# Kernel optimization log

Hardware: AMD Instinct MI355X
Metric: run time of the kernel (lower is better)

Reference implementation:

```python
import jax, jax.numpy as jnp
import numpy as np

N, C, E = 100000, 128, 600000
H = C // 2  # 64


def setup_inputs() -> dict:
    key = jax.random.key(0)
    k1, k2, k3, k4, k5, k6, k7, k8 = jax.random.split(key, 8)
    z_in = jax.random.normal(k1, (N, C), dtype=jnp.float32)
    z_out = jax.random.normal(k2, (N, C), dtype=jnp.float32)
    z_self = jax.random.normal(k3, (N, C), dtype=jnp.float32)
    edge_index = jax.random.randint(k4, (2, E), 0, N, dtype=jnp.int64)
    # MLP params: Linear(C, C//2) -> ELU -> (Dropout eval=no-op) -> Linear(C//2, 1)
    lim1 = 1.0 / np.sqrt(C)
    W1 = jax.random.uniform(k5, (C, H), minval=-lim1, maxval=lim1, dtype=jnp.float32)
    b1 = jax.random.uniform(k6, (H,), minval=-lim1, maxval=lim1, dtype=jnp.float32)
    lim2 = 1.0 / np.sqrt(H)
    W2 = jax.random.uniform(k7, (H, 1), minval=-lim2, maxval=lim2, dtype=jnp.float32)
    b2 = jax.random.uniform(k8, (1,), minval=-lim2, maxval=lim2, dtype=jnp.float32)
    return {"z_in": z_in, "z_out": z_out, "z_self": z_self,
            "edge_index": edge_index, "W1": W1, "b1": b1, "W2": W2, "b2": b2}


def reference(z_in, z_out, z_self, edge_index, W1, b1, W2, b2):
    v1 = z_out + z_self                       # [N, C]
    v2 = z_in + z_self                        # [N, C]
    value = v1[edge_index[0]] * v2[edge_index[1]]  # [E, C] gather + elementwise product
    h = jax.nn.elu(value @ W1 + b1)           # [E, H]; dropout is identity at eval
    logits = h @ W2 + b2                      # [E, 1]
    return jax.nn.sigmoid(logits)
```

## Files before the change

### kernel.cpp

```cpp
#include <hip/hip_runtime.h>
#include <hip/hip_bf16.h>

typedef __attribute__((ext_vector_type(8))) short short8;
typedef __attribute__((ext_vector_type(4))) float f32x4;

__device__ __forceinline__ unsigned short f2bf(float f) {
    unsigned u = __float_as_uint(f);
    u += 0x7fffu + ((u >> 16) & 1u);
    return (unsigned short)(u >> 16);
}

__device__ __forceinline__ unsigned bfmul_trunc(unsigned a, unsigned b) {
    float al = __uint_as_float(a << 16);
    float ah = __uint_as_float(a & 0xffff0000u);
    float bl = __uint_as_float(b << 16);
    float bh = __uint_as_float(b & 0xffff0000u);
    unsigned pl = __float_as_uint(al * bl);
    unsigned ph = __float_as_uint(ah * bh);
    return __builtin_amdgcn_perm(ph, pl, 0x07060302u);
}

__device__ __forceinline__ unsigned pack_trunc(float lo, float hi) {
    return __builtin_amdgcn_perm(__float_as_uint(hi), __float_as_uint(lo), 0x07060302u);
}

__global__ __launch_bounds__(256) void prep_kernel(
    const f32x4* __restrict__ zin, const f32x4* __restrict__ zout,
    const f32x4* __restrict__ zself,
    ushort4* __restrict__ v1b, ushort4* __restrict__ v2b, int n4)
{
    const int base = blockIdx.x * 1024 + threadIdx.x;
    const bool full = (blockIdx.x + 1) * 1024 <= n4;
    if (full) {
        f32x4 o[4], s[4], z[4];
#pragma unroll
        for (int u = 0; u < 4; u++) {
            const int i = base + u * 256;
            o[u] = __builtin_nontemporal_load(zout + i);
            s[u] = __builtin_nontemporal_load(zself + i);
            z[u] = __builtin_nontemporal_load(zin + i);
        }
#pragma unroll
        for (int u = 0; u < 4; u++) {
            const int i = base + u * 256;
            ushort4 a, b;
            a.x = f2bf(o[u].x + s[u].x); a.y = f2bf(o[u].y + s[u].y);
            a.z = f2bf(o[u].z + s[u].z); a.w = f2bf(o[u].w + s[u].w);
            b.x = f2bf(z[u].x + s[u].x); b.y = f2bf(z[u].y + s[u].y);
            b.z = f2bf(z[u].z + s[u].z); b.w = f2bf(z[u].w + s[u].w);
            v1b[i] = a; v2b[i] = b;
        }
    } else {
#pragma unroll
        for (int u = 0; u < 4; u++) {
            const int i = base + u * 256;
            if (i < n4) {
                f32x4 o = __builtin_nontemporal_load(zout + i);
                f32x4 s = __builtin_nontemporal_load(zself + i);
                f32x4 z = __builtin_nontemporal_load(zin + i);
                ushort4 a, b;
                a.x = f2bf(o.x + s.x); a.y = f2bf(o.y + s.y);
                a.z = f2bf(o.z + s.z); a.w = f2bf(o.w + s.w);
                b.x = f2bf(z.x + s.x); b.y = f2bf(z.y + s.y);
                b.z = f2bf(z.z + s.z); b.w = f2bf(z.w + s.w);
                v1b[i] = a; v2b[i] = b;
            }
        }
    }
}

__global__ __launch_bounds__(256, 4) void edge_pipe(
    const unsigned short* __restrict__ v1b, const unsigned short* __restrict__ v2b,
    const int* __restrict__ idx,
    const float* __restrict__ W1, const float* __restrict__ b1,
    const float* __restrict__ W2, const float* __restrict__ b2,
    float* __restrict__ out, int E, int ntiles)
{
    __shared__ __align__(16) unsigned short ldsW[16 * 64 * 8];

    const int tid  = threadIdx.x;
    const int wave = tid >> 6;
    const int lane = tid & 63;
    const int nn = lane & 15;
    const int q  = lane >> 4;

#pragma unroll
    for (int i = 0; i < 4; i++) {
        int p = tid * 4 + i;
        int f = p >> 6, l = p & 63;
        int kc = f >> 2, jt = f & 3, lq = (l >> 4) & 3, ln = l & 15;
        const float* wp = W1 + (size_t)(kc * 32 + lq * 8) * 64 + jt * 16 + ln;
        uint4 wv;
        wv.x = (unsigned)f2bf(wp[0 * 64]) | ((unsigned)f2bf(wp[1 * 64]) << 16);
        wv.y = (unsigned)f2bf(wp[2 * 64]) | ((unsigned)f2bf(wp[3 * 64]) << 16);
        wv.z = (unsigned)f2bf(wp[4 * 64]) | ((unsigned)f2bf(wp[5 * 64]) << 16);
        wv.w = (unsigned)f2bf(wp[6 * 64]) | ((unsigned)f2bf(wp[7 * 64]) << 16);
        *(uint4*)&ldsW[p * 8] = wv;
    }
    __syncthreads();

    float bias1[4], w2v[4];
#pragma unroll
    for (int jt = 0; jt < 4; jt++) {
        bias1[jt] = b1[jt * 16 + nn];
        w2v[jt]   = W2[jt * 16 + nn];
    }
    const float b2v = b2[0];

    const int nwaves = gridDim.x * 4;
    int tile = blockIdx.x * 4 + wave;
    if (tile >= ntiles) return;
    const int* __restrict__ idxE = idx + E;

    const int e0  = min(tile * 16 + nn, E - 1);
    const int t1  = tile + nwaves;
    const int tc1 = (t1 < ntiles) ? t1 : tile;
    const int e1  = min(tc1 * 16 + nn, E - 1);
    const int src0 = __builtin_nontemporal_load(idx  + e0);
    const int dst0 = __builtin_nontemporal_load(idxE + e0);
    int srcn = __builtin_nontemporal_load(idx  + e1);
    int dstn = __builtin_nontemporal_load(idxE + e1);

    uint4 a[4], b[4];
    {
        const uint4* p1 = (const uint4*)(v1b + (size_t)src0 * 128);
        const uint4* p2 = (const uint4*)(v2b + (size_t)dst0 * 128);
#pragma unroll
        for (int kc = 0; kc < 4; kc++) { a[kc] = p1[kc * 4 + q]; b[kc] = p2[kc * 4 + q]; }
    }

    for (; tile < ntiles; tile += nwaves) {
        const int t2  = tile + 2 * nwaves;
        const int tc2 = (t2 < ntiles) ? t2 : tile;
        const int e2  = min(tc2 * 16 + nn, E - 1);
        const int src2 = __builtin_nontemporal_load(idx  + e2);
        const int dst2 = __builtin_nontemporal_load(idxE + e2);

        short8 Af[4];
#pragma unroll
        for (int kc = 0; kc < 4; kc++) {
            uint4 p;
            p.x = bfmul_trunc(a[kc].x, b[kc].x);
            p.y = bfmul_trunc(a[kc].y, b[kc].y);
            p.z = bfmul_trunc(a[kc].z, b[kc].z);
            p.w = bfmul_trunc(a[kc].w, b[kc].w);
            Af[kc] = __builtin_bit_cast(short8, p);
        }

        {
            const uint4* p1 = (const uint4*)(v1b + (size_t)srcn * 128);
            const uint4* p2 = (const uint4*)(v2b + (size_t)dstn * 128);
#pragma unroll
            for (int kc = 0; kc < 4; kc++) { a[kc] = p1[kc * 4 + q]; b[kc] = p2[kc * 4 + q]; }
        }
        srcn = src2; dstn = dst2;

        f32x4 acc[4];
#pragma unroll
        for (int jt = 0; jt < 4; jt++) acc[jt] = (f32x4){0.f, 0.f, 0.f, 0.f};
#pragma unroll
        for (int kc = 0; kc < 4; kc++) {
#pragma unroll
            for (int jt = 0; jt < 4; jt++) {
                short8 Bf = *(const short8*)&ldsW[((kc * 4 + jt) * 64 + lane) * 8];
                acc[jt] = __builtin_amdgcn_mfma_f32_16x16x32_bf16(Af[kc], Bf, acc[jt], 0, 0, 0);
            }
        }

        float ps[4];
#pragma unroll
        for (int r = 0; r < 4; r++) {
            float s = 0.f;
#pragma unroll
            for (int jt = 0; jt < 4; jt++) {
                float h = acc[jt][r] + bias1[jt];
                h = (h > 0.f) ? h : (__expf(h) - 1.f);
                s += h * w2v[jt];
            }
            ps[r] = s;
        }
#pragma unroll
        for (int off = 1; off < 16; off <<= 1) {
#pragma unroll
            for (int r = 0; r < 4; r++)
                ps[r] += __shfl_xor(ps[r], off, 64);
        }
        if (nn == 0) {
#pragma unroll
            for (int r = 0; r < 4; r++) {
                int e = tile * 16 + q * 4 + r;
                if (e < E) {
                    float x = ps[r] + b2v;
                    __builtin_nontemporal_store(1.f / (1.f + __expf(-x)), out + e);
                }
            }
        }
    }
}

__global__ __launch_bounds__(256) void edge_f32(
    const float* __restrict__ zin, const float* __restrict__ zout,
    const float* __restrict__ zself,
    const int* __restrict__ idx,
    const float* __restrict__ W1, const float* __restrict__ b1,
    const float* __restrict__ W2, const float* __restrict__ b2,
    float* __restrict__ out, int E, int ntiles)
{
    const int wave = threadIdx.x >> 6;
    const int lane = threadIdx.x & 63;
    const int nn = lane & 15;
    const int q  = lane >> 4;

    short8 Bf[4][4];
#pragma unroll
    for (int kc = 0; kc < 4; kc++)
#pragma unroll
        for (int jt = 0; jt < 4; jt++) {
            short8 v;
#pragma unroll
            for (int t = 0; t < 8; t++)
                v[t] = (short)f2bf(W1[(kc * 32 + q * 8 + t) * 64 + jt * 16 + nn]);
            Bf[kc][jt] = v;
        }
    float bias1[4], w2v[4];
#pragma unroll
    for (int jt = 0; jt < 4; jt++) {
        bias1[jt] = b1[jt * 16 + nn];
        w2v[jt]   = W2[jt * 16 + nn];
    }
    const float b2v = b2[0];

    const int nwaves = gridDim.x * 4;
    for (int tile = blockIdx.x * 4 + wave; tile < ntiles; tile += nwaves) {
        const int ebase = tile * 16;
        const int ee  = min(ebase + nn, E - 1);
        const int src = idx[ee];
        const int dst = idx[E + ee];

        short8 Af[4];
        const float* po  = zout  + (size_t)src * 128 + q * 8;
        const float* ps1 = zself + (size_t)src * 128 + q * 8;
        const float* pi  = zin   + (size_t)dst * 128 + q * 8;
        const float* ps2 = zself + (size_t)dst * 128 + q * 8;
#pragma unroll
        for (int kc = 0; kc < 4; kc++) {
            float4 oa = *(const float4*)(po  + kc * 32), ob = *(const float4*)(po  + kc * 32 + 4);
            float4 sa = *(const float4*)(ps1 + kc * 32), sb = *(const float4*)(ps1 + kc * 32 + 4);
            float4 ia = *(const float4*)(pi  + kc * 32), ib = *(const float4*)(pi  + kc * 32 + 4);
            float4 ta = *(const float4*)(ps2 + kc * 32), tb = *(const float4*)(ps2 + kc * 32 + 4);
            uint4 p;
            p.x = pack_trunc((oa.x + sa.x) * (ia.x + ta.x), (oa.y + sa.y) * (ia.y + ta.y));
            p.y = pack_trunc((oa.z + sa.z) * (ia.z + ta.z), (oa.w + sa.w) * (ia.w + ta.w));
            p.z = pack_trunc((ob.x + sb.x) * (ib.x + tb.x), (ob.y + sb.y) * (ib.y + tb.y));
            p.w = pack_trunc((ob.z + sb.z) * (ib.z + tb.z), (ob.w + sb.w) * (ib.w + tb.w));
            Af[kc] = __builtin_bit_cast(short8, p);
        }

        f32x4 acc[4];
#pragma unroll
        for (int jt = 0; jt < 4; jt++) acc[jt] = (f32x4){0.f, 0.f, 0.f, 0.f};
#pragma unroll
        for (int kc = 0; kc < 4; kc++)
#pragma unroll
            for (int jt = 0; jt < 4; jt++)
                acc[jt] = __builtin_amdgcn_mfma_f32_16x16x32_bf16(Af[kc], Bf[kc][jt], acc[jt], 0, 0, 0);

        float ps[4];
#pragma unroll
        for (int r = 0; r < 4; r++) {
            float s = 0.f;
#pragma unroll
            for (int jt = 0; jt < 4; jt++) {
                float h = acc[jt][r] + bias1[jt];
                h = (h > 0.f) ? h : (__expf(h) - 1.f);
                s += h * w2v[jt];
            }
            ps[r] = s;
        }
#pragma unroll
        for (int off = 1; off < 16; off <<= 1) {
#pragma unroll
            for (int r = 0; r < 4; r++)
                ps[r] += __shfl_xor(ps[r], off, 64);
        }
        if (nn == 0) {
#pragma unroll
            for (int r = 0; r < 4; r++) {
                int e = ebase + q * 4 + r;
                if (e < E) {
                    float x = ps[r] + b2v;
                    out[e] = 1.f / (1.f + __expf(-x));
                }
            }
        }
    }
}

extern "C" void kernel_launch(void* const* d_in, const int* in_sizes, int n_in,
                              void* d_out, int out_size, void* d_ws, size_t ws_size,
                              hipStream_t stream)
{
    const float* zin   = (const float*)d_in[0];
    const float* zout  = (const float*)d_in[1];
    const float* zself = (const float*)d_in[2];
    const int*   idx   = (const int*)d_in[3];
    const float* W1    = (const float*)d_in[4];
    const float* b1    = (const float*)d_in[5];
    const float* W2    = (const float*)d_in[6];
    const float* b2    = (const float*)d_in[7];
    float* out = (float*)d_out;

    const int NC = in_sizes[0];
    const int E  = in_sizes[3] / 2;
    const int ntiles = (E + 15) / 16;
    const size_t need = (size_t)NC * 4;

    if (ws_size >= need) {
        unsigned short* v1b = (unsigned short*)d_ws;
        unsigned short* v2b = v1b + NC;
        const int n4 = NC / 4;
        const int nblocks = (n4 + 1023) / 1024;
        prep_kernel<<<nblocks, 256, 0, stream>>>(
            (const f32x4*)zin, (const f32x4*)zout, (const f32x4*)zself,
            (ushort4*)v1b, (ushort4*)v2b, n4);

        const int cap = 2048;
        int iters = (ntiles + cap * 4 - 1) / (cap * 4);
        if (iters < 1) iters = 1;
        int eblocks = (ntiles + iters * 4 - 1) / (iters * 4);
        edge_pipe<<<eblocks, 256, 0, stream>>>(
            v1b, v2b, idx, W1, b1, W2, b2, out, E, ntiles);
    } else {
        edge_f32<<<2048, 256, 0, stream>>>(
            zin, zout, zself, idx, W1, b1, W2, b2, out, E, ntiles);
    }
}
```

Baseline: 225.9 us.

## Bucket edges by source node range before gathering to improve cache locality

Adds a scatter pass that partitions edges into 16 buckets by source-node range, writing (src, dst, edge id) records. The edge kernel then assigns blocks to buckets so that concurrently running waves gather from a narrower slice of v1b, aiming for better L2/MALL reuse. Outputs are written back through the stored edge id. The cost is two extra kernel launches, an extra read of the indices, a 16-byte-per-edge record write and read, and scattered output stores.

```diff
diff --git a/kernel.cpp b/kernel.cpp
--- a/kernel.cpp
+++ b/kernel.cpp
@@ -3,6 +3,9 @@
 
 typedef __attribute__((ext_vector_type(8))) short short8;
 typedef __attribute__((ext_vector_type(4))) float f32x4;
+typedef __attribute__((ext_vector_type(4))) int   i32x4;
+
+#define NBKT 16
 
 __device__ __forceinline__ unsigned short f2bf(float f) {
     unsigned u = __float_as_uint(f);
@@ -69,12 +72,47 @@
     }
 }
 
-__global__ __launch_bounds__(256, 4) void edge_pipe(
+__global__ void k_init(int* ctl, int cap)
+{
+    if (threadIdx.x < NBKT) ctl[threadIdx.x] = threadIdx.x * cap;
+}
+
+__global__ __launch_bounds__(256) void k_scatter(
+    const int* __restrict__ idx, int E, int slice, int CH,
+    int* __restrict__ ctl, int cap, i32x4* __restrict__ rec)
+{
+    __shared__ int hist[NBKT], base[NBKT];
+    const int c0 = blockIdx.x * CH;
+    const int c1 = min(c0 + CH, E);
+    if (threadIdx.x < NBKT) hist[threadIdx.x] = 0;
+    __syncthreads();
+    for (int e = c0 + threadIdx.x; e < c1; e += 256) {
+        int b = min(idx[e] / slice, NBKT - 1);
+        atomicAdd(&hist[b], 1);
+    }
+    __syncthreads();
+    if (threadIdx.x < NBKT) {
+        int c = hist[threadIdx.x];
+        base[threadIdx.x] = c ? atomicAdd(&ctl[threadIdx.x], c)
+                              : threadIdx.x * cap;
+        hist[threadIdx.x] = 0;
+    }
+    __syncthreads();
+    for (int e = c0 + threadIdx.x; e < c1; e += 256) {
+        int s = idx[e], d = idx[E + e];
+        int b = min(s / slice, NBKT - 1);
+        int p = base[b] + atomicAdd(&hist[b], 1);
+        i32x4 r; r[0] = s; r[1] = d; r[2] = e; r[3] = 0;
+        __builtin_nontemporal_store(r, rec + p);
+    }
+}
+
+__global__ __launch_bounds__(256, 4) void edge_bkt(
     const unsigned short* __restrict__ v1b, const unsigned short* __restrict__ v2b,
-    const int* __restrict__ idx,
+    const i32x4* __restrict__ rec, const int* __restrict__ ctl, int cap,
     const float* __restrict__ W1, const float* __restrict__ b1,
     const float* __restrict__ W2, const float* __restrict__ b2,
-    float* __restrict__ out, int E, int ntiles)
+    float* __restrict__ out)
 {
     __shared__ __align__(16) unsigned short ldsW[16 * 64 * 8];
 
@@ -107,6 +145,144 @@
     }
     const float b2v = b2[0];
 
+    const int nw  = (gridDim.x >> 3) * 4;
+    const int wi0 = (blockIdx.x >> 3) * 4 + wave;
+    const int bkt0 = blockIdx.x & 7;
+
+    for (int ph = 0; ph < 2; ph++) {
+        const int bk = bkt0 + ph * 8;
+        const int bbase = bk * cap;
+        const int bcnt  = ctl[bk] - bbase;
+        const int btiles = (bcnt + 15) >> 4;
+        int t = ph ? (nw - 1 - wi0) : wi0;
+        if (t >= btiles) continue;
+
+        auto recAt = [&](int tt) -> i32x4 {
+            int r = min(tt * 16 + nn, bcnt - 1);
+            return __builtin_nontemporal_load(rec + bbase + r);
+        };
+
+        i32x4 r0 = recAt(t);
+        const int tA = t + nw;
+        i32x4 r1 = recAt(tA < btiles ? tA : t);
+        int eo_cur = r0[2];
+        int srcn = r1[0], dstn = r1[1], eon = r1[2];
+
+        uint4 a[4], b[4];
+        {
+            const uint4* p1 = (const uint4*)(v1b + (size_t)r0[0] * 128);
+            const uint4* p2 = (const uint4*)(v2b + (size_t)r0[1] * 128);
+#pragma unroll
+            for (int kc = 0; kc < 4; kc++) { a[kc] = p1[kc * 4 + q]; b[kc] = p2[kc * 4 + q]; }
+        }
+
+        for (; t < btiles; t += nw) {
+            const int t2 = t + 2 * nw;
+            i32x4 r2 = recAt(t2 < btiles ? t2 : t);
+
+            short8 Af[4];
+#pragma unroll
+            for (int kc = 0; kc < 4; kc++) {
+                uint4 p;
+                p.x = bfmul_trunc(a[kc].x, b[kc].x);
+                p.y = bfmul_trunc(a[kc].y, b[kc].y);
+                p.z = bfmul_trunc(a[kc].z, b[kc].z);
+                p.w = bfmul_trunc(a[kc].w, b[kc].w);
+                Af[kc] = __builtin_bit_cast(short8, p);
+            }
+
+            {
+                const uint4* p1 = (const uint4*)(v1b + (size_t)srcn * 128);
+                const uint4* p2 = (const uint4*)(v2b + (size_t)dstn * 128);
+#pragma unroll
+                for (int kc = 0; kc < 4; kc++) { a[kc] = p1[kc * 4 + q]; b[kc] = p2[kc * 4 + q]; }
+            }
+            const int eo_st = eo_cur;
+            eo_cur = eon;
+            srcn = r2[0]; dstn = r2[1]; eon = r2[2];
+
+            f32x4 acc[4];
+#pragma unroll
+            for (int jt = 0; jt < 4; jt++) acc[jt] = (f32x4){0.f, 0.f, 0.f, 0.f};
+#pragma unroll
+            for (int kc = 0; kc < 4; kc++) {
+#pragma unroll
+                for (int jt = 0; jt < 4; jt++) {
+                    short8 Bf = *(const short8*)&ldsW[((kc * 4 + jt) * 64 + lane) * 8];
+                    acc[jt] = __builtin_amdgcn_mfma_f32_16x16x32_bf16(Af[kc], Bf, acc[jt], 0, 0, 0);
+                }
+            }
+
+            float ps[4];
+#pragma unroll
+            for (int r = 0; r < 4; r++) {
+                float s = 0.f;
+#pragma unroll
+                for (int jt = 0; jt < 4; jt++) {
+                    float h = acc[jt][r] + bias1[jt];
+                    h = (h > 0.f) ? h : (__expf(h) - 1.f);
+                    s += h * w2v[jt];
+                }
+                ps[r] = s;
+            }
+#pragma unroll
+            for (int off = 1; off < 16; off <<= 1) {
+#pragma unroll
+                for (int r = 0; r < 4; r++)
+                    ps[r] += __shfl_xor(ps[r], off, 64);
+            }
+            int eoq[4];
+#pragma unroll
+            for (int r = 0; r < 4; r++) eoq[r] = __shfl(eo_st, (q << 2) + r, 16);
+            if (nn == 0) {
+#pragma unroll
+                for (int r = 0; r < 4; r++) {
+                    float x = ps[r] + b2v;
+                    __builtin_nontemporal_store(1.f / (1.f + __expf(-x)), out + eoq[r]);
+                }
+            }
+        }
+    }
+}
+
+__global__ __launch_bounds__(256, 4) void edge_pipe(
+    const unsigned short* __restrict__ v1b, const unsigned short* __restrict__ v2b,
+    const int* __restrict__ idx,
+    const float* __restrict__ W1, const float* __restrict__ b1,
+    const float* __restrict__ W2, const float* __restrict__ b2,
+    float* __restrict__ out, int E, int ntiles)
+{
+    __shared__ __align__(16) unsigned short ldsW[16 * 64 * 8];
+
+    const int tid  = threadIdx.x;
+    const int wave = tid >> 6;
+    const int lane = tid & 63;
+    const int nn = lane & 15;
+    const int q  = lane >> 4;
+
+#pragma unroll
+    for (int i = 0; i < 4; i++) {
+        int p = tid * 4 + i;
+        int f = p >> 6, l = p & 63;
+        int kc = f >> 2, jt = f & 3, lq = (l >> 4) & 3, ln = l & 15;
+        const float* wp = W1 + (size_t)(kc * 32 + lq * 8) * 64 + jt * 16 + ln;
+        uint4 wv;
+        wv.x = (unsigned)f2bf(wp[0 * 64]) | ((unsigned)f2bf(wp[1 * 64]) << 16);
+        wv.y = (unsigned)f2bf(wp[2 * 64]) | ((unsigned)f2bf(wp[3 * 64]) << 16);
+        wv.z = (unsigned)f2bf(wp[4 * 64]) | ((unsigned)f2bf(wp[5 * 64]) << 16);
+        wv.w = (unsigned)f2bf(wp[6 * 64]) | ((unsigned)f2bf(wp[7 * 64]) << 16);
+        *(uint4*)&ldsW[p * 8] = wv;
+    }
+    __syncthreads();
+
+    float bias1[4], w2v[4];
+#pragma unroll
+    for (int jt = 0; jt < 4; jt++) {
+        bias1[jt] = b1[jt * 16 + nn];
+        w2v[jt]   = W2[jt * 16 + nn];
+    }
+    const float b2v = b2[0];
+
     const int nwaves = gridDim.x * 4;
     int tile = blockIdx.x * 4 + wave;
     if (tile >= ntiles) return;
@@ -146,7 +322,6 @@
             p.w = bfmul_trunc(a[kc].w, b[kc].w);
             Af[kc] = __builtin_bit_cast(short8, p);
         }
-
         {
             const uint4* p1 = (const uint4*)(v1b + (size_t)srcn * 128);
             const uint4* p2 = (const uint4*)(v2b + (size_t)dstn * 128);
@@ -312,20 +487,48 @@
 
     const int NC = in_sizes[0];
     const int E  = in_sizes[3] / 2;
+    const int N  = NC / 128;
     const int ntiles = (E + 15) / 16;
-    const size_t need = (size_t)NC * 4;
-
-    if (ws_size >= need) {
+
+    const int slice = (N + NBKT - 1) / NBKT;
+    const int cap   = E / NBKT + 2048;
+
+    const size_t need1 = (size_t)NC * 4;
+    const size_t off_rec = need1;
+    const size_t off_ctl = off_rec + (size_t)NBKT * cap * 16;
+    const size_t need2 = off_ctl + 256;
+
+    if (ws_size >= need2) {
+        unsigned short* v1b = (unsigned short*)d_ws;
+        unsigned short* v2b = v1b + NC;
+        i32x4* rec = (i32x4*)((char*)d_ws + off_rec);
+        int*   ctl = (int*)((char*)d_ws + off_ctl);
+        const int n4 = NC / 4;
+        prep_kernel<<<(n4 + 1023) / 1024, 256, 0, stream>>>(
+            (const f32x4*)zin, (const f32x4*)zout, (const f32x4*)zself,
+            (ushort4*)v1b, (ushort4*)v2b, n4);
+        k_init<<<1, 64, 0, stream>>>(ctl, cap);
+        const int SB = 256;
+        const int CH = (E + SB - 1) / SB;
+        k_scatter<<<SB, 256, 0, stream>>>(idx, E, slice, CH, ctl, cap, rec);
+
+        int iters = (ntiles + 8191) / 8192; if (iters < 1) iters = 1;
+        int nwavesT = (ntiles + iters - 1) / iters;
+        int wpg = (nwavesT + 7) / 8;
+        int bpg = (wpg + 3) / 4;
+        if (bpg < 1) bpg = 1;
+        if (bpg > 256) bpg = 256;
+        edge_bkt<<<bpg * 8, 256, 0, stream>>>(
+            v1b, v2b, rec, ctl, cap, W1, b1, W2, b2, out);
+    } else if (ws_size >= need1) {
         unsigned short* v1b = (unsigned short*)d_ws;
         unsigned short* v2b = v1b + NC;
         const int n4 = NC / 4;
-        const int nblocks = (n4 + 1023) / 1024;
-        prep_kernel<<<nblocks, 256, 0, stream>>>(
+        prep_kernel<<<(n4 + 1023) / 1024, 256, 0, stream>>>(
             (const f32x4*)zin, (const f32x4*)zout, (const f32x4*)zself,
             (ushort4*)v1b, (ushort4*)v2b, n4);
-
-        const int cap = 2048;
-        int iters = (ntiles + cap * 4 - 1) / (cap * 4);
+        const int cap2 = 2048;
+        int iters = (ntiles + cap2 * 4 - 1) / (cap2 * 4);
         if (iters < 1) iters = 1;
         int eblocks = (ntiles + iters * 4 - 1) / (iters * 4);
         edge_pipe<<<eblocks, 256, 0, stream>>>(
```

Result: slower. 263.2 us (+16.5%).

## Quantize node features to int8 with per-row scales to halve gather traffic

Applied to the files above, without the earlier changes.

The prep kernel now stores v1 and v2 as int8 with one absmax scale per row, instead of bf16. The edge kernel gathers 8-byte chunks instead of 16-byte chunks, plus two scale loads per edge. It then dequantizes each product as int8*int8*scale before packing to bf16 for the MFMA. This halves the random-gather bytes per edge and shrinks the prep kernel's writes, which matters because the random gathers dominate the cost. The trade-offs are more ALU work per element for unpacking and conversion, extra scalar scale loads, and lower precision from per-row 8-bit quantization.

```diff
diff --git a/kernel.cpp b/kernel.cpp
--- a/kernel.cpp
+++ b/kernel.cpp
@@ -10,67 +10,70 @@
     return (unsigned short)(u >> 16);
 }
 
-__device__ __forceinline__ unsigned bfmul_trunc(unsigned a, unsigned b) {
-    float al = __uint_as_float(a << 16);
-    float ah = __uint_as_float(a & 0xffff0000u);
-    float bl = __uint_as_float(b << 16);
-    float bh = __uint_as_float(b & 0xffff0000u);
-    unsigned pl = __float_as_uint(al * bl);
-    unsigned ph = __float_as_uint(ah * bh);
-    return __builtin_amdgcn_perm(ph, pl, 0x07060302u);
-}
-
 __device__ __forceinline__ unsigned pack_trunc(float lo, float hi) {
     return __builtin_amdgcn_perm(__float_as_uint(hi), __float_as_uint(lo), 0x07060302u);
 }
 
-__global__ __launch_bounds__(256) void prep_kernel(
+
+__global__ __launch_bounds__(256) void prep_i8(
     const f32x4* __restrict__ zin, const f32x4* __restrict__ zout,
     const f32x4* __restrict__ zself,
-    ushort4* __restrict__ v1b, ushort4* __restrict__ v2b, int n4)
+    unsigned* __restrict__ q1, unsigned* __restrict__ q2,
+    float* __restrict__ s1, float* __restrict__ s2, int N)
 {
-    const int base = blockIdx.x * 1024 + threadIdx.x;
-    const bool full = (blockIdx.x + 1) * 1024 <= n4;
-    if (full) {
-        f32x4 o[4], s[4], z[4];
-#pragma unroll
-        for (int u = 0; u < 4; u++) {
-            const int i = base + u * 256;
-            o[u] = __builtin_nontemporal_load(zout + i);
-            s[u] = __builtin_nontemporal_load(zself + i);
-            z[u] = __builtin_nontemporal_load(zin + i);
-        }
-#pragma unroll
-        for (int u = 0; u < 4; u++) {
-            const int i = base + u * 256;
-            ushort4 a, b;
-            a.x = f2bf(o[u].x + s[u].x); a.y = f2bf(o[u].y + s[u].y);
-            a.z = f2bf(o[u].z + s[u].z); a.w = f2bf(o[u].w + s[u].w);
-            b.x = f2bf(z[u].x + s[u].x); b.y = f2bf(z[u].y + s[u].y);
-            b.z = f2bf(z[u].z + s[u].z); b.w = f2bf(z[u].w + s[u].w);
-            v1b[i] = a; v2b[i] = b;
-        }
-    } else {
-#pragma unroll
-        for (int u = 0; u < 4; u++) {
-            const int i = base + u * 256;
-            if (i < n4) {
-                f32x4 o = __builtin_nontemporal_load(zout + i);
-                f32x4 s = __builtin_nontemporal_load(zself + i);
-                f32x4 z = __builtin_nontemporal_load(zin + i);
-                ushort4 a, b;
-                a.x = f2bf(o.x + s.x); a.y = f2bf(o.y + s.y);
-                a.z = f2bf(o.z + s.z); a.w = f2bf(o.w + s.w);
-                b.x = f2bf(z.x + s.x); b.y = f2bf(z.y + s.y);
-                b.z = f2bf(z.z + s.z); b.w = f2bf(z.w + s.w);
-                v1b[i] = a; v2b[i] = b;
-            }
-        }
-    }
-}
-
-__global__ __launch_bounds__(256, 4) void edge_pipe(
-    const unsigned short* __restrict__ v1b, const unsigned short* __restrict__ v2b,
+    const int lane = threadIdx.x & 63;
+    const int wave = threadIdx.x >> 6;
+    const int h    = lane >> 5;
+    const int l32  = lane & 31;
+    const int row  = blockIdx.x * 8 + wave * 2 + h;
+    if (row >= N) return;
+    const size_t rb = (size_t)row * 32 + l32;
+
+    f32x4 o = __builtin_nontemporal_load(zout  + rb);
+    f32x4 s = __builtin_nontemporal_load(zself + rb);
+    f32x4 z = __builtin_nontemporal_load(zin   + rb);
+    float v1[4] = {o.x + s.x, o.y + s.y, o.z + s.z, o.w + s.w};
+    float v2[4] = {z.x + s.x, z.y + s.y, z.z + s.z, z.w + s.w};
+
+    float m1 = fmaxf(fmaxf(fabsf(v1[0]), fabsf(v1[1])),
+                     fmaxf(fabsf(v1[2]), fabsf(v1[3])));
+    float m2 = fmaxf(fmaxf(fabsf(v2[0]), fabsf(v2[1])),
+                     fmaxf(fabsf(v2[2]), fabsf(v2[3])));
+#pragma unroll
+    for (int off = 1; off < 32; off <<= 1) {
+        m1 = fmaxf(m1, __shfl_xor(m1, off, 64));
+        m2 = fmaxf(m2, __shfl_xor(m2, off, 64));
+    }
+    m1 = fmaxf(m1, 1e-20f);
+    m2 = fmaxf(m2, 1e-20f);
+    const float i1 = 127.0f / m1, i2 = 127.0f / m2;
+
+    int qa[4], qb[4];
+#pragma unroll
+    for (int j = 0; j < 4; j++) {
+        qa[j] = (int)rintf(v1[j] * i1);
+        qb[j] = (int)rintf(v2[j] * i2);
+    }
+    unsigned wa = (unsigned)(qa[0] & 255) | ((unsigned)(qa[1] & 255) << 8) |
+                  ((unsigned)(qa[2] & 255) << 16) | ((unsigned)qa[3] << 24);
+    unsigned wb = (unsigned)(qb[0] & 255) | ((unsigned)(qb[1] & 255) << 8) |
+                  ((unsigned)(qb[2] & 255) << 16) | ((unsigned)qb[3] << 24);
+    q1[rb] = wa; q2[rb] = wb;
+    if (l32 == 0) {
+        s1[row] = m1 * (1.0f / 127.0f);
+        s2[row] = m2 * (1.0f / 127.0f);
+    }
+}
+
+__device__ __forceinline__ float pmul(unsigned aw, unsigned bw, int sh) {
+    int a = (int)(signed char)(aw >> sh);
+    int b = (int)(signed char)(bw >> sh);
+    return (float)(a * b);
+}
+
+__global__ __launch_bounds__(256, 4) void edge_pipe_i8(
+    const unsigned* __restrict__ q1, const unsigned* __restrict__ q2,
+    const float* __restrict__ s1, const float* __restrict__ s2,
     const int* __restrict__ idx,
     const float* __restrict__ W1, const float* __restrict__ b1,
     const float* __restrict__ W2, const float* __restrict__ b2,
@@ -121,10 +124,12 @@
     int srcn = __builtin_nontemporal_load(idx  + e1);
     int dstn = __builtin_nontemporal_load(idxE + e1);
 
-    uint4 a[4], b[4];
+    float sN_a = s1[src0], sN_b = s2[dst0];
+
+    uint2 a[4], b[4];
     {
-        const uint4* p1 = (const uint4*)(v1b + (size_t)src0 * 128);
-        const uint4* p2 = (const uint4*)(v2b + (size_t)dst0 * 128);
+        const uint2* p1 = (const uint2*)q1 + (size_t)src0 * 16;
+        const uint2* p2 = (const uint2*)q2 + (size_t)dst0 * 16;
 #pragma unroll
         for (int kc = 0; kc < 4; kc++) { a[kc] = p1[kc * 4 + q]; b[kc] = p2[kc * 4 + q]; }
     }
@@ -136,22 +141,28 @@
         const int src2 = __builtin_nontemporal_load(idx  + e2);
         const int dst2 = __builtin_nontemporal_load(idxE + e2);
 
+        const float s12 = sN_a * sN_b;
         short8 Af[4];
 #pragma unroll
         for (int kc = 0; kc < 4; kc++) {
             uint4 p;
-            p.x = bfmul_trunc(a[kc].x, b[kc].x);
-            p.y = bfmul_trunc(a[kc].y, b[kc].y);
-            p.z = bfmul_trunc(a[kc].z, b[kc].z);
-            p.w = bfmul_trunc(a[kc].w, b[kc].w);
+            p.x = pack_trunc(pmul(a[kc].x, b[kc].x,  0) * s12,
+                             pmul(a[kc].x, b[kc].x,  8) * s12);
+            p.y = pack_trunc(pmul(a[kc].x, b[kc].x, 16) * s12,
+                             pmul(a[kc].x, b[kc].x, 24) * s12);
+            p.z = pack_trunc(pmul(a[kc].y, b[kc].y,  0) * s12,
+                             pmul(a[kc].y, b[kc].y,  8) * s12);
+            p.w = pack_trunc(pmul(a[kc].y, b[kc].y, 16) * s12,
+                             pmul(a[kc].y, b[kc].y, 24) * s12);
             Af[kc] = __builtin_bit_cast(short8, p);
         }
 
         {
-            const uint4* p1 = (const uint4*)(v1b + (size_t)srcn * 128);
-            const uint4* p2 = (const uint4*)(v2b + (size_t)dstn * 128);
+            const uint2* p1 = (const uint2*)q1 + (size_t)srcn * 16;
+            const uint2* p2 = (const uint2*)q2 + (size_t)dstn * 16;
 #pragma unroll
             for (int kc = 0; kc < 4; kc++) { a[kc] = p1[kc * 4 + q]; b[kc] = p2[kc * 4 + q]; }
+            sN_a = s1[srcn]; sN_b = s2[dstn];
         }
         srcn = src2; dstn = dst2;
 
@@ -311,25 +322,26 @@
     float* out = (float*)d_out;
 
     const int NC = in_sizes[0];
+    const int N  = NC / 128;
     const int E  = in_sizes[3] / 2;
     const int ntiles = (E + 15) / 16;
-    const size_t need = (size_t)NC * 4;
+    const size_t need = (size_t)NC * 2 + (size_t)N * 8;
 
     if (ws_size >= need) {
-        unsigned short* v1b = (unsigned short*)d_ws;
-        unsigned short* v2b = v1b + NC;
-        const int n4 = NC / 4;
-        const int nblocks = (n4 + 1023) / 1024;
-        prep_kernel<<<nblocks, 256, 0, stream>>>(
+        unsigned* q1 = (unsigned*)d_ws;
+        unsigned* q2 = q1 + NC / 4;
+        float* s1 = (float*)((char*)d_ws + (size_t)NC * 2);
+        float* s2 = s1 + N;
+        prep_i8<<<(N + 7) / 8, 256, 0, stream>>>(
             (const f32x4*)zin, (const f32x4*)zout, (const f32x4*)zself,
-            (ushort4*)v1b, (ushort4*)v2b, n4);
+            q1, q2, s1, s2, N);
 
         const int cap = 2048;
         int iters = (ntiles + cap * 4 - 1) / (cap * 4);
         if (iters < 1) iters = 1;
         int eblocks = (ntiles + iters * 4 - 1) / (iters * 4);
-        edge_pipe<<<eblocks, 256, 0, stream>>>(
-            v1b, v2b, idx, W1, b1, W2, b2, out, E, ntiles);
+        edge_pipe_i8<<<eblocks, 256, 0, stream>>>(
+            q1, q2, s1, s2, idx, W1, b1, W2, b2, out, E, ntiles);
     } else {
         edge_f32<<<2048, 256, 0, stream>>>(
             zin, zout, zself, idx, W1, b1, W2, b2, out, E, ntiles);
```

Measured after the change: 231.6 us. 1.03x slower.
